# Kernel tuning notes

Hardware: AMD Instinct MI355X
Metric: run time of the kernel (lower is better)

Reference implementation:

```python
import jax, jax.numpy as jnp
import numpy as np

B, T_IN, T_DEC = 64, 64, 47   # batch, encoder len, decoder steps (max_length_output-1)
V, E, H = 32000, 512, 1024    # vocab, embed dim, hidden


def setup_inputs() -> dict:
    key = jax.random.key(0)
    ks = jax.random.split(key, 12)
    s = 0.02
    return {
        "tokens": jax.random.randint(ks[0], (B, T_DEC), 0, V),
        "memory": jax.random.normal(ks[1], (B, T_IN, H), jnp.float32),
        "enc_h": jax.random.normal(ks[2], (B, H), jnp.float32),
        "enc_c": jax.random.normal(ks[3], (B, H), jnp.float32),
        "emb": jax.random.normal(ks[4], (V, E), jnp.float32) * s,
        "Wm": jax.random.normal(ks[5], (H, H), jnp.float32) * s,      # Luong memory_layer (no bias)
        "Wa": jax.random.normal(ks[6], (2 * H, H), jnp.float32) * s,  # attention_layer (no bias)
        "lstm_k": jax.random.normal(ks[7], (E + H, 4 * H), jnp.float32) * s,
        "lstm_r": jax.random.normal(ks[8], (H, 4 * H), jnp.float32) * s,
        "lstm_b": jnp.zeros((4 * H,), jnp.float32),
        "fc_w": jax.random.normal(ks[9], (H, V), jnp.float32) * s,
        "fc_b": jnp.zeros((V,), jnp.float32),
    }


def reference(tokens, memory, enc_h, enc_c, emb, Wm, Wa, lstm_k, lstm_r, lstm_b, fc_w, fc_b):
    # Luong attention keys: memory projected once, outside the decode loop
    keys_att = jnp.einsum('bth,hu->btu', memory, Wm)          # [B,T_in,H]
    xs = jnp.swapaxes(emb[tokens], 0, 1)                      # [T_dec,B,E] teacher-forced inputs

    def step(carry, x_t):
        h, c, attn = carry
        # AttentionWrapper: cell input = concat(embedding, prev attention)
        inp = jnp.concatenate([x_t, attn], axis=-1)           # [B,E+H]
        z = inp @ lstm_k + h @ lstm_r + lstm_b                # [B,4H], Keras gate order i,f,g,o
        i, f, g, o = jnp.split(z, 4, axis=-1)
        c2 = jax.nn.sigmoid(f) * c + jax.nn.sigmoid(i) * jnp.tanh(g)
        h2 = jax.nn.sigmoid(o) * jnp.tanh(c2)
        # Luong score = query . keys; full-length memory (no mask needed)
        score = jnp.einsum('bh,bth->bt', h2, keys_att)        # [B,T_in]
        align = jax.nn.softmax(score, axis=-1)
        ctx = jnp.einsum('bt,bth->bh', align, memory)         # [B,H]
        attn2 = jnp.concatenate([h2, ctx], axis=-1) @ Wa      # attention_layer -> [B,H]
        logits = attn2 @ fc_w + fc_b                          # output_layer -> [B,V]
        return (h2, c2, attn2), logits

    init = (enc_h, enc_c, jnp.zeros_like(enc_h))
    _, ys = jax.lax.scan(step, init, xs)                      # [T_dec,B,V]
    return jnp.swapaxes(ys, 0, 1)                             # [B,T_dec,V]
```

## Files before the change

kernel.cpp:

```cpp
#include <hip/hip_runtime.h>

typedef __bf16 bf16;
typedef __bf16 bf16x8 __attribute__((ext_vector_type(8)));
typedef __bf16 bf16x4 __attribute__((ext_vector_type(4)));
typedef float  f32x4  __attribute__((ext_vector_type(4)));

__device__ __forceinline__ void async16(const bf16* g, bf16* l) {
  __builtin_amdgcn_global_load_lds(
      (__attribute__((address_space(1))) void*)(void*)(const_cast<bf16*>(g)),
      (__attribute__((address_space(3))) void*)(void*)l,
      16, 0, 0);
}


__global__ void cvt_bf16(const float* __restrict__ s, bf16* __restrict__ d, int n) {
  int i = blockIdx.x * blockDim.x + threadIdx.x;
  int stride = gridDim.x * blockDim.x;
  for (int k = i; k < n; k += stride) d[k] = (bf16)s[k];
}

__global__ void transpose_to_bf16(const float* __restrict__ src, bf16* __restrict__ dst,
                                  int R, int C) {
  __shared__ float tile[32][33];
  int c0 = blockIdx.x * 32, r0 = blockIdx.y * 32;
  int tx = threadIdx.x, ty = threadIdx.y;
#pragma unroll
  for (int k = 0; k < 32; k += 8)
    tile[ty + k][tx] = src[(size_t)(r0 + ty + k) * C + (c0 + tx)];
  __syncthreads();
#pragma unroll
  for (int k = 0; k < 32; k += 8)
    dst[(size_t)(c0 + ty + k) * R + (r0 + tx)] = (bf16)tile[tx][ty + k];
}

__global__ void gather_emb(const int* __restrict__ tokens, const float* __restrict__ emb,
                           bf16* __restrict__ X) {
  int r = blockIdx.x;
  int tid = threadIdx.x;
  if (r < 3008) {
    int t = r >> 6, b = r & 63;
    int tok = tokens[b * 47 + t];
    const float* e = emb + (size_t)tok * 512;
    for (int k = tid; k < 512; k += 128) X[(size_t)r * 512 + k] = (bf16)e[k];
  } else {
    for (int k = tid; k < 512; k += 128) X[(size_t)r * 512 + k] = (bf16)0.f;
  }
}

__global__ void init_state(const float* __restrict__ enc_h, const float* __restrict__ enc_c,
                           bf16* __restrict__ S0, float* __restrict__ cbuf) {
  int i = blockIdx.x * 256 + threadIdx.x;
  int b = i >> 10, u = i & 1023;
  S0[(size_t)b * 2048 + u]        = (bf16)enc_h[i];
  S0[(size_t)b * 2048 + 1024 + u] = (bf16)0.f;
  cbuf[i] = enc_c[i];
}

template <int MODE, int SWAP = 0>
__global__ __launch_bounds__(256) void gemm_bt(
    const bf16* __restrict__ A, int lda,
    const bf16* __restrict__ B, int ldb, int K,
    void* __restrict__ C, int ldc,
    const void* __restrict__ aux) {
  __shared__ bf16 As[128 * 32];
  __shared__ bf16 Bs[128 * 32];
  const int tid = threadIdx.x;
  const int wave = tid >> 6, lane = tid & 63;
  const int wm = wave >> 1, wn = wave & 1;
  const int quad = lane >> 4, l16 = lane & 15;
  const size_t r0 = (size_t)(SWAP ? blockIdx.x : blockIdx.y) * 128;
  const size_t c0 = (size_t)(SWAP ? blockIdx.y : blockIdx.x) * 128;

  f32x4 acc[4][4] = {};

  for (int k0 = 0; k0 < K; k0 += 32) {
#pragma unroll
    for (int j = 0; j < 2; ++j) {
      int seg = j * 256 + tid;
      int row = seg >> 2, ks = seg & 3;
      async16(A + (r0 + row) * (size_t)lda + k0 + ks * 8, As + seg * 8);
    }
#pragma unroll
    for (int j = 0; j < 2; ++j) {
      int seg = j * 256 + tid;
      int row = seg >> 2, ks = seg & 3;
      async16(B + (c0 + row) * (size_t)ldb + k0 + ks * 8, Bs + seg * 8);
    }
    __syncthreads();
    bf16x8 af[4], bfr[4];
#pragma unroll
    for (int mi = 0; mi < 4; ++mi)
      af[mi] = *(const bf16x8*)(As + (wm * 64 + mi * 16 + l16) * 32 + quad * 8);
#pragma unroll
    for (int ni = 0; ni < 4; ++ni)
      bfr[ni] = *(const bf16x8*)(Bs + (wn * 64 + ni * 16 + l16) * 32 + quad * 8);
#pragma unroll
    for (int mi = 0; mi < 4; ++mi)
#pragma unroll
      for (int ni = 0; ni < 4; ++ni)
        acc[mi][ni] = __builtin_amdgcn_mfma_f32_16x16x32_bf16(af[mi], bfr[ni], acc[mi][ni], 0, 0, 0);
    __syncthreads();
  }

#pragma unroll
  for (int mi = 0; mi < 4; ++mi)
#pragma unroll
    for (int ni = 0; ni < 4; ++ni)
#pragma unroll
      for (int reg = 0; reg < 4; ++reg) {
        size_t r = r0 + wm * 64 + mi * 16 + quad * 4 + reg;
        size_t c = c0 + wn * 64 + ni * 16 + l16;
        float v = acc[mi][ni][reg];
        if (MODE == 0) {
          ((bf16*)C)[r * ldc + c] = (bf16)v;
        } else if (MODE == 1) {
          if (c < 1024) v += (float)((const bf16*)aux)[r * 1024 + c];
          ((bf16*)C)[r * ldc + c] = (bf16)v;
        } else if (MODE == 2) {
          v += ((const float*)aux)[c];
          ((float*)C)[r * ldc + c] = v;
        } else if (MODE == 3) {
          if (r < 3008) {
            size_t t = r >> 6, b = r & 63;
            ((float*)C)[(b * 47 + t) * (size_t)32000 + c] = v + ((const float*)aux)[c];
          }
        } else {
          ((float*)C)[r * ldc + c] = v;
        }
      }
}

template <int KK>
__global__ __launch_bounds__(256) void step_gates2(
    const bf16* __restrict__ Sin,
    const bf16* __restrict__ Bt,
    int ldb,
    const float* __restrict__ pct,
    float* __restrict__ cbuf,
    bf16* __restrict__ HC_t)
{
  __shared__ bf16 Bs[16 * 2048];
  __shared__ float zs[64 * 16];
  const int tid = threadIdx.x;
  const int p = blockIdx.x;
  const int wave = tid >> 6, lane = tid & 63;
  const int quad = lane >> 4, l16 = lane & 15;

  constexpr int NSEG = KK / 8;
  constexpr int SH = (KK == 2048) ? 8 : 7;
#pragma unroll
  for (int i = 0; i < 16 * NSEG / 256; ++i) {
    int seg = i * 256 + tid;
    int n = seg >> SH;
    int ko = seg & (NSEG - 1);
    int gkb = (ko * 16) ^ ((n & 7) << 4);
    int ng = (n >> 2) * 1024 + p * 4 + (n & 3);
    async16(Bt + (size_t)ng * ldb + (gkb >> 1), Bs + n * 2048 + ko * 8);
  }

  const bf16* arow = Sin + (size_t)(wave * 16 + l16) * 2048 + quad * 8;
  const char* bbase = (const char*)Bs + l16 * 4096;
  const int bswz = (l16 & 7) << 4;
  __syncthreads();

  f32x4 acc0 = {}, acc1 = {};
  constexpr int KS = KK / 32;
#pragma unroll 8
  for (int ks = 0; ks < KS; ks += 2) {
    bf16x8 b0 = *(const bf16x8*)(bbase + ((ks * 64 + quad * 16) ^ bswz));
    bf16x8 a0 = *(const bf16x8*)(arow + (size_t)ks * 32);
    acc0 = __builtin_amdgcn_mfma_f32_16x16x32_bf16(a0, b0, acc0, 0, 0, 0);
    bf16x8 b1 = *(const bf16x8*)(bbase + (((ks + 1) * 64 + quad * 16) ^ bswz));
    bf16x8 a1 = *(const bf16x8*)(arow + (size_t)(ks + 1) * 32);
    acc1 = __builtin_amdgcn_mfma_f32_16x16x32_bf16(a1, b1, acc1, 0, 0, 0);
  }

  {
    int gcol = (l16 >> 2) * 1024 + p * 4 + (l16 & 3);
#pragma unroll
    for (int reg = 0; reg < 4; ++reg) {
      int row = wave * 16 + quad * 4 + reg;
      zs[row * 16 + l16] = acc0[reg] + acc1[reg] + pct[(size_t)row * 4096 + gcol];
    }
  }
  __syncthreads();

  {
    int b = tid >> 2, s = tid & 3;
    int j = p * 4 + s;
    float iv = zs[b * 16 + s];
    float fv = zs[b * 16 + 4 + s];
    float gv = zs[b * 16 + 8 + s];
    float ov = zs[b * 16 + 12 + s];
    float c_old = cbuf[b * 1024 + j];
    float ig = 1.f / (1.f + __expf(-iv));
    float fg = 1.f / (1.f + __expf(-fv));
    float og = 1.f / (1.f + __expf(-ov));
    float c2 = fg * c_old + ig * tanhf(gv);
    float h2 = og * tanhf(c2);
    cbuf[b * 1024 + j] = c2;
    HC_t[(size_t)b * 2048 + j] = (bf16)h2;
  }
}

__global__ __launch_bounds__(256) void step_attn2(
    bf16* __restrict__ HC_t,
    const float* __restrict__ keys,
    const bf16* __restrict__ memB)
{
  __shared__ float sm[64];
  const int b = blockIdx.x;
  const int tid = threadIdx.x;
  const int wave = tid >> 6, lane = tid & 63;

  float hv[16];
  {
    const bf16* hp = HC_t + (size_t)b * 2048 + lane * 16;
    bf16x8 h0 = *(const bf16x8*)(hp);
    bf16x8 h1 = *(const bf16x8*)(hp + 8);
#pragma unroll
    for (int e = 0; e < 8; ++e) { hv[e] = (float)h0[e]; hv[8 + e] = (float)h1[e]; }
  }

#pragma unroll 4
  for (int ii = 0; ii < 16; ++ii) {
    int it = wave * 16 + ii;
    const float* krow = keys + ((size_t)b * 64 + it) * 1024 + lane * 16;
    f32x4 k0 = *(const f32x4*)(krow);
    f32x4 k1 = *(const f32x4*)(krow + 4);
    f32x4 k2 = *(const f32x4*)(krow + 8);
    f32x4 k3 = *(const f32x4*)(krow + 12);
    float pr = hv[0] * k0[0] + hv[1] * k0[1] + hv[2] * k0[2] + hv[3] * k0[3]
             + hv[4] * k1[0] + hv[5] * k1[1] + hv[6] * k1[2] + hv[7] * k1[3]
             + hv[8] * k2[0] + hv[9] * k2[1] + hv[10] * k2[2] + hv[11] * k2[3]
             + hv[12] * k3[0] + hv[13] * k3[1] + hv[14] * k3[2] + hv[15] * k3[3];
#pragma unroll
    for (int off = 32; off > 0; off >>= 1) pr += __shfl_xor(pr, off);
    if (lane == 0) sm[it] = pr;
  }
  __syncthreads();

  if (tid < 64) {
    float s = sm[tid];
    float mx = s;
#pragma unroll
    for (int off = 32; off > 0; off >>= 1) mx = fmaxf(mx, __shfl_xor(mx, off));
    float e = __expf(s - mx);
    float sum = e;
#pragma unroll
    for (int off = 32; off > 0; off >>= 1) sum += __shfl_xor(sum, off);
    sm[tid] = e / sum;
  }
  __syncthreads();

  int u0 = tid * 4;
  float a0 = 0.f, a1 = 0.f, a2 = 0.f, a3 = 0.f;
#pragma unroll 4
  for (int i = 0; i < 64; ++i) {
    float al = sm[i];
    bf16x4 m4 = *(const bf16x4*)(memB + ((size_t)b * 64 + i) * 1024 + u0);
    a0 += al * (float)m4[0];
    a1 += al * (float)m4[1];
    a2 += al * (float)m4[2];
    a3 += al * (float)m4[3];
  }
  bf16* so = HC_t + (size_t)b * 2048 + 1024 + u0;
  so[0] = (bf16)a0;
  so[1] = (bf16)a1;
  so[2] = (bf16)a2;
  so[3] = (bf16)a3;
}


extern "C" void kernel_launch(void* const* d_in, const int* in_sizes, int n_in,
                              void* d_out, int out_size, void* d_ws, size_t ws_size,
                              hipStream_t stream) {
  const int*   tokens = (const int*)d_in[0];
  const float* memory = (const float*)d_in[1];
  const float* enc_h  = (const float*)d_in[2];
  const float* enc_c  = (const float*)d_in[3];
  const float* emb    = (const float*)d_in[4];
  const float* Wm     = (const float*)d_in[5];
  const float* Wa     = (const float*)d_in[6];
  const float* lstm_k = (const float*)d_in[7];
  const float* lstm_r = (const float*)d_in[8];
  const float* lstm_b = (const float*)d_in[9];
  const float* fc_w   = (const float*)d_in[10];
  const float* fc_b   = (const float*)d_in[11];
  float* out = (float*)d_out;

  char* ob = (char*)d_out;
  size_t off = 0;
  auto alloc_o = [&](size_t bytes) { char* q = ob + off; off += bytes; return q; };
  bf16*  memB    = (bf16*)alloc_o(8388608);
  float* keys    = (float*)alloc_o(16777216);
  bf16*  WaB     = (bf16*)alloc_o(4194304);
  bf16*  WmT     = (bf16*)alloc_o(2097152);
  bf16*  KpT     = (bf16*)alloc_o(8388608);
  bf16*  KxT     = (bf16*)alloc_o(4194304);
  bf16*  RT      = (bf16*)alloc_o(8388608);
  bf16*  WaT     = (bf16*)alloc_o(4194304);
  bf16*  X       = (bf16*)alloc_o(3145728);
  bf16*  W12T    = (bf16*)alloc_o(16777216);
  bf16*  S0      = (bf16*)alloc_o(262144);
  float* cbuf    = (float*)alloc_o(262144);
  bf16*  HC      = (bf16*)alloc_o(12582912);
  float* precomp = (float*)alloc_o(50331648);

  char* wb = (char*)d_ws;
  bf16* fcwT  = (bf16*)(wb);
  bf16* attnb = (bf16*)(wb + 65536000);

  dim3 tb(32, 8);

  cvt_bf16<<<2048, 256, 0, stream>>>(memory, memB, 4194304);
  cvt_bf16<<<2048, 256, 0, stream>>>(Wa, WaB, 2097152);
  transpose_to_bf16<<<dim3(32, 32), tb, 0, stream>>>(Wm, WmT, 1024, 1024);
  transpose_to_bf16<<<dim3(128, 32), tb, 0, stream>>>(lstm_k + (size_t)512 * 4096, KpT, 1024, 4096);
  transpose_to_bf16<<<dim3(128, 16), tb, 0, stream>>>(lstm_k, KxT, 512, 4096);
  transpose_to_bf16<<<dim3(128, 32), tb, 0, stream>>>(lstm_r, RT, 1024, 4096);
  transpose_to_bf16<<<dim3(32, 64), tb, 0, stream>>>(Wa, WaT, 2048, 1024);
  transpose_to_bf16<<<dim3(1000, 32), tb, 0, stream>>>(fc_w, fcwT, 1024, 32000);
  gather_emb<<<3072, 128, 0, stream>>>(tokens, emb, X);
  init_state<<<256, 256, 0, stream>>>(enc_h, enc_c, S0, cbuf);

  gemm_bt<4><<<dim3(8, 32), 256, 0, stream>>>(memB, 1024, WmT, 1024, 1024, keys, 1024, nullptr);
  gemm_bt<1><<<dim3(16, 32), 256, 0, stream>>>(KpT, 1024, WaB, 1024, 1024, W12T, 2048, RT);
  gemm_bt<2><<<dim3(32, 24), 256, 0, stream>>>(X, 512, KxT, 512, 512, precomp, 4096, lstm_b);

  for (int t = 0; t < 47; ++t) {
    const bf16* Sin = (t == 0) ? S0 : (HC + (size_t)(t - 1) * 131072);
    bf16* HC_t = HC + (size_t)t * 131072;
    const float* pct = precomp + (size_t)t * 262144;
    if (t == 0)
      step_gates2<1024><<<256, 256, 0, stream>>>(Sin, RT, 1024, pct, cbuf, HC_t);
    else
      step_gates2<2048><<<256, 256, 0, stream>>>(Sin, W12T, 2048, pct, cbuf, HC_t);
    step_attn2<<<64, 256, 0, stream>>>(HC_t, keys, memB);
  }

  gemm_bt<0><<<dim3(8, 24), 256, 0, stream>>>(HC, 2048, WaT, 2048, 2048, attnb, 1024, nullptr);
  gemm_bt<3, 1><<<dim3(24, 250), 256, 0, stream>>>(attnb, 1024, fcwT, 1024, 1024, out, 32000, fc_b);

  (void)in_sizes; (void)n_in; (void)out_size; (void)ws_size;
}
```

Measured before the change: 2.425 ms.

## Fuse decoder loop into one persistent kernel with atomic-flag grid barriers

Result: slower. 3.244 ms (+33.8%).

```diff
diff --git a/kernel.cpp b/kernel.cpp
--- a/kernel.cpp
+++ b/kernel.cpp
@@ -47,16 +47,16 @@
   }
 }
 
-__global__ void init_state(const float* __restrict__ enc_h, const float* __restrict__ enc_c,
-                           bf16* __restrict__ S0, float* __restrict__ cbuf) {
+__global__ void init_state(const float* __restrict__ enc_h, bf16* __restrict__ S0,
+                           unsigned int* __restrict__ flags) {
   int i = blockIdx.x * 256 + threadIdx.x;
   int b = i >> 10, u = i & 1023;
   S0[(size_t)b * 2048 + u]        = (bf16)enc_h[i];
   S0[(size_t)b * 2048 + 1024 + u] = (bf16)0.f;
-  cbuf[i] = enc_c[i];
-}
-
-template <int MODE, int SWAP = 0>
+  if (blockIdx.x == 0 && threadIdx.x < 128) flags[threadIdx.x] = 0u;
+}
+
+template <int MODE>
 __global__ __launch_bounds__(256) void gemm_bt(
     const bf16* __restrict__ A, int lda,
     const bf16* __restrict__ B, int ldb, int K,
@@ -68,8 +68,8 @@
   const int wave = tid >> 6, lane = tid & 63;
   const int wm = wave >> 1, wn = wave & 1;
   const int quad = lane >> 4, l16 = lane & 15;
-  const size_t r0 = (size_t)(SWAP ? blockIdx.x : blockIdx.y) * 128;
-  const size_t c0 = (size_t)(SWAP ? blockIdx.y : blockIdx.x) * 128;
+  const size_t r0 = (size_t)blockIdx.y * 128;
+  const size_t c0 = (size_t)blockIdx.x * 128;
 
   f32x4 acc[4][4] = {};
 
@@ -130,145 +130,186 @@
       }
 }
 
-template <int KK>
-__global__ __launch_bounds__(256) void step_gates2(
-    const bf16* __restrict__ Sin,
-    const bf16* __restrict__ Bt,
-    int ldb,
-    const float* __restrict__ pct,
-    float* __restrict__ cbuf,
-    bf16* __restrict__ HC_t)
+__global__ __launch_bounds__(256) void decoder_fused(
+    const bf16* __restrict__ S0,
+    const bf16* __restrict__ W12T,
+    const bf16* __restrict__ RT,
+    const float* __restrict__ precomp,
+    const float* __restrict__ enc_c,
+    const float* __restrict__ keys,
+    const bf16* __restrict__ memB,
+    bf16* __restrict__ HC,
+    unsigned int* __restrict__ flags)
 {
   __shared__ bf16 Bs[16 * 2048];
   __shared__ float zs[64 * 16];
+  __shared__ float sm[64];
+
   const int tid = threadIdx.x;
   const int p = blockIdx.x;
   const int wave = tid >> 6, lane = tid & 63;
   const int quad = lane >> 4, l16 = lane & 15;
-
-  constexpr int NSEG = KK / 8;
-  constexpr int SH = (KK == 2048) ? 8 : 7;
-#pragma unroll
-  for (int i = 0; i < 16 * NSEG / 256; ++i) {
+  const int growB = (l16 >> 2) * 1024 + p * 4 + (l16 & 3);
+
+#pragma unroll
+  for (int i = 0; i < 16; ++i) {
     int seg = i * 256 + tid;
-    int n = seg >> SH;
-    int ko = seg & (NSEG - 1);
+    int n = seg >> 8;
+    int ko = seg & 255;
     int gkb = (ko * 16) ^ ((n & 7) << 4);
     int ng = (n >> 2) * 1024 + p * 4 + (n & 3);
-    async16(Bt + (size_t)ng * ldb + (gkb >> 1), Bs + n * 2048 + ko * 8);
-  }
-
-  const bf16* arow = Sin + (size_t)(wave * 16 + l16) * 2048 + quad * 8;
+    async16(W12T + (size_t)ng * 2048 + (gkb >> 1), Bs + n * 2048 + ko * 8);
+  }
+
+  float c_reg;
+  {
+    int b = tid >> 2, s = tid & 3;
+    c_reg = enc_c[b * 1024 + p * 4 + s];
+  }
+
   const char* bbase = (const char*)Bs + l16 * 4096;
   const int bswz = (l16 & 7) << 4;
+
   __syncthreads();
 
-  f32x4 acc0 = {}, acc1 = {};
-  constexpr int KS = KK / 32;
+  for (int t = 0; t < 47; ++t) {
+    const bf16* Sin = t ? (HC + (size_t)(t - 1) * 131072) : S0;
+    bf16* HC_t = HC + (size_t)t * 131072;
+    const float* pct = precomp + (size_t)t * 262144;
+    const bf16* arow = Sin + (size_t)(wave * 16 + l16) * 2048 + quad * 8;
+
+    f32x4 acc0 = {}, acc1 = {};
+    if (t == 0) {
+      const bf16* brow = RT + (size_t)growB * 1024 + quad * 8;
 #pragma unroll 8
-  for (int ks = 0; ks < KS; ks += 2) {
-    bf16x8 b0 = *(const bf16x8*)(bbase + ((ks * 64 + quad * 16) ^ bswz));
-    bf16x8 a0 = *(const bf16x8*)(arow + (size_t)ks * 32);
-    acc0 = __builtin_amdgcn_mfma_f32_16x16x32_bf16(a0, b0, acc0, 0, 0, 0);
-    bf16x8 b1 = *(const bf16x8*)(bbase + (((ks + 1) * 64 + quad * 16) ^ bswz));
-    bf16x8 a1 = *(const bf16x8*)(arow + (size_t)(ks + 1) * 32);
-    acc1 = __builtin_amdgcn_mfma_f32_16x16x32_bf16(a1, b1, acc1, 0, 0, 0);
-  }
-
-  {
-    int gcol = (l16 >> 2) * 1024 + p * 4 + (l16 & 3);
+      for (int ks = 0; ks < 32; ks += 2) {
+        bf16x8 b0 = *(const bf16x8*)(brow + ks * 32);
+        bf16x8 a0 = *(const bf16x8*)(arow + (size_t)ks * 32);
+        acc0 = __builtin_amdgcn_mfma_f32_16x16x32_bf16(a0, b0, acc0, 0, 0, 0);
+        bf16x8 b1 = *(const bf16x8*)(brow + (ks + 1) * 32);
+        bf16x8 a1 = *(const bf16x8*)(arow + (size_t)(ks + 1) * 32);
+        acc1 = __builtin_amdgcn_mfma_f32_16x16x32_bf16(a1, b1, acc1, 0, 0, 0);
+      }
+    } else {
+#pragma unroll 8
+      for (int ks = 0; ks < 64; ks += 2) {
+        bf16x8 b0 = *(const bf16x8*)(bbase + ((ks * 64 + quad * 16) ^ bswz));
+        bf16x8 a0 = *(const bf16x8*)(arow + (size_t)ks * 32);
+        acc0 = __builtin_amdgcn_mfma_f32_16x16x32_bf16(a0, b0, acc0, 0, 0, 0);
+        bf16x8 b1 = *(const bf16x8*)(bbase + (((ks + 1) * 64 + quad * 16) ^ bswz));
+        bf16x8 a1 = *(const bf16x8*)(arow + (size_t)(ks + 1) * 32);
+        acc1 = __builtin_amdgcn_mfma_f32_16x16x32_bf16(a1, b1, acc1, 0, 0, 0);
+      }
+    }
+
 #pragma unroll
     for (int reg = 0; reg < 4; ++reg) {
       int row = wave * 16 + quad * 4 + reg;
-      zs[row * 16 + l16] = acc0[reg] + acc1[reg] + pct[(size_t)row * 4096 + gcol];
-    }
-  }
-  __syncthreads();
-
-  {
-    int b = tid >> 2, s = tid & 3;
-    int j = p * 4 + s;
-    float iv = zs[b * 16 + s];
-    float fv = zs[b * 16 + 4 + s];
-    float gv = zs[b * 16 + 8 + s];
-    float ov = zs[b * 16 + 12 + s];
-    float c_old = cbuf[b * 1024 + j];
-    float ig = 1.f / (1.f + __expf(-iv));
-    float fg = 1.f / (1.f + __expf(-fv));
-    float og = 1.f / (1.f + __expf(-ov));
-    float c2 = fg * c_old + ig * tanhf(gv);
-    float h2 = og * tanhf(c2);
-    cbuf[b * 1024 + j] = c2;
-    HC_t[(size_t)b * 2048 + j] = (bf16)h2;
-  }
-}
-
-__global__ __launch_bounds__(256) void step_attn2(
-    bf16* __restrict__ HC_t,
-    const float* __restrict__ keys,
-    const bf16* __restrict__ memB)
-{
-  __shared__ float sm[64];
-  const int b = blockIdx.x;
-  const int tid = threadIdx.x;
-  const int wave = tid >> 6, lane = tid & 63;
-
-  float hv[16];
-  {
-    const bf16* hp = HC_t + (size_t)b * 2048 + lane * 16;
-    bf16x8 h0 = *(const bf16x8*)(hp);
-    bf16x8 h1 = *(const bf16x8*)(hp + 8);
-#pragma unroll
-    for (int e = 0; e < 8; ++e) { hv[e] = (float)h0[e]; hv[8 + e] = (float)h1[e]; }
-  }
+      zs[row * 16 + l16] = acc0[reg] + acc1[reg] + pct[(size_t)row * 4096 + growB];
+    }
+    __syncthreads();
+
+    {
+      int b = tid >> 2, s = tid & 3;
+      float iv = zs[b * 16 + s];
+      float fv = zs[b * 16 + 4 + s];
+      float gv = zs[b * 16 + 8 + s];
+      float ov = zs[b * 16 + 12 + s];
+      float ig = 1.f / (1.f + __expf(-iv));
+      float fg = 1.f / (1.f + __expf(-fv));
+      float og = 1.f / (1.f + __expf(-ov));
+      float c2 = fg * c_reg + ig * tanhf(gv);
+      float h2 = og * tanhf(c2);
+      c_reg = c2;
+      HC_t[(size_t)b * 2048 + p * 4 + s] = (bf16)h2;
+    }
+    __syncthreads();
+    if (tid == 0) {
+      __threadfence();
+      __hip_atomic_fetch_add(&flags[t], 1u, __ATOMIC_RELAXED, __HIP_MEMORY_SCOPE_AGENT);
+    }
+
+    if (p < 64) {
+      if (tid == 0) {
+        while (__hip_atomic_load(&flags[t], __ATOMIC_RELAXED, __HIP_MEMORY_SCOPE_AGENT) < 256u)
+          __builtin_amdgcn_s_sleep(2);
+        __threadfence();
+      }
+      __syncthreads();
+
+      const int b = p;
+      float hv[16];
+      {
+        const bf16* hp = HC_t + (size_t)b * 2048 + lane * 16;
+        bf16x8 h0 = *(const bf16x8*)(hp);
+        bf16x8 h1 = *(const bf16x8*)(hp + 8);
+#pragma unroll
+        for (int e = 0; e < 8; ++e) { hv[e] = (float)h0[e]; hv[8 + e] = (float)h1[e]; }
+      }
 
 #pragma unroll 4
-  for (int ii = 0; ii < 16; ++ii) {
-    int it = wave * 16 + ii;
-    const float* krow = keys + ((size_t)b * 64 + it) * 1024 + lane * 16;
-    f32x4 k0 = *(const f32x4*)(krow);
-    f32x4 k1 = *(const f32x4*)(krow + 4);
-    f32x4 k2 = *(const f32x4*)(krow + 8);
-    f32x4 k3 = *(const f32x4*)(krow + 12);
-    float pr = hv[0] * k0[0] + hv[1] * k0[1] + hv[2] * k0[2] + hv[3] * k0[3]
-             + hv[4] * k1[0] + hv[5] * k1[1] + hv[6] * k1[2] + hv[7] * k1[3]
-             + hv[8] * k2[0] + hv[9] * k2[1] + hv[10] * k2[2] + hv[11] * k2[3]
-             + hv[12] * k3[0] + hv[13] * k3[1] + hv[14] * k3[2] + hv[15] * k3[3];
-#pragma unroll
-    for (int off = 32; off > 0; off >>= 1) pr += __shfl_xor(pr, off);
-    if (lane == 0) sm[it] = pr;
-  }
-  __syncthreads();
-
-  if (tid < 64) {
-    float s = sm[tid];
-    float mx = s;
-#pragma unroll
-    for (int off = 32; off > 0; off >>= 1) mx = fmaxf(mx, __shfl_xor(mx, off));
-    float e = __expf(s - mx);
-    float sum = e;
-#pragma unroll
-    for (int off = 32; off > 0; off >>= 1) sum += __shfl_xor(sum, off);
-    sm[tid] = e / sum;
-  }
-  __syncthreads();
-
-  int u0 = tid * 4;
-  float a0 = 0.f, a1 = 0.f, a2 = 0.f, a3 = 0.f;
+      for (int ii = 0; ii < 16; ++ii) {
+        int it = wave * 16 + ii;
+        const float* krow = keys + ((size_t)b * 64 + it) * 1024 + lane * 16;
+        f32x4 k0 = *(const f32x4*)(krow);
+        f32x4 k1 = *(const f32x4*)(krow + 4);
+        f32x4 k2 = *(const f32x4*)(krow + 8);
+        f32x4 k3 = *(const f32x4*)(krow + 12);
+        float pr = hv[0] * k0[0] + hv[1] * k0[1] + hv[2] * k0[2] + hv[3] * k0[3]
+                 + hv[4] * k1[0] + hv[5] * k1[1] + hv[6] * k1[2] + hv[7] * k1[3]
+                 + hv[8] * k2[0] + hv[9] * k2[1] + hv[10] * k2[2] + hv[11] * k2[3]
+                 + hv[12] * k3[0] + hv[13] * k3[1] + hv[14] * k3[2] + hv[15] * k3[3];
+#pragma unroll
+        for (int off = 32; off > 0; off >>= 1) pr += __shfl_xor(pr, off);
+        if (lane == 0) sm[it] = pr;
+      }
+      __syncthreads();
+
+      if (tid < 64) {
+        float s = sm[tid];
+        float mx = s;
+#pragma unroll
+        for (int off = 32; off > 0; off >>= 1) mx = fmaxf(mx, __shfl_xor(mx, off));
+        float e = __expf(s - mx);
+        float sum = e;
+#pragma unroll
+        for (int off = 32; off > 0; off >>= 1) sum += __shfl_xor(sum, off);
+        sm[tid] = e / sum;
+      }
+      __syncthreads();
+
+      int u0 = tid * 4;
+      float a0 = 0.f, a1 = 0.f, a2 = 0.f, a3 = 0.f;
 #pragma unroll 4
-  for (int i = 0; i < 64; ++i) {
-    float al = sm[i];
-    bf16x4 m4 = *(const bf16x4*)(memB + ((size_t)b * 64 + i) * 1024 + u0);
-    a0 += al * (float)m4[0];
-    a1 += al * (float)m4[1];
-    a2 += al * (float)m4[2];
-    a3 += al * (float)m4[3];
-  }
-  bf16* so = HC_t + (size_t)b * 2048 + 1024 + u0;
-  so[0] = (bf16)a0;
-  so[1] = (bf16)a1;
-  so[2] = (bf16)a2;
-  so[3] = (bf16)a3;
+      for (int i = 0; i < 64; ++i) {
+        float al = sm[i];
+        bf16x4 m4 = *(const bf16x4*)(memB + ((size_t)b * 64 + i) * 1024 + u0);
+        a0 += al * (float)m4[0];
+        a1 += al * (float)m4[1];
+        a2 += al * (float)m4[2];
+        a3 += al * (float)m4[3];
+      }
+      bf16* so = HC_t + (size_t)b * 2048 + 1024 + u0;
+      so[0] = (bf16)a0;
+      so[1] = (bf16)a1;
+      so[2] = (bf16)a2;
+      so[3] = (bf16)a3;
+      __syncthreads();
+      if (tid == 0) {
+        __threadfence();
+        __hip_atomic_fetch_add(&flags[64 + t], 1u, __ATOMIC_RELAXED, __HIP_MEMORY_SCOPE_AGENT);
+      }
+    }
+
+    if (t < 46) {
+      if (tid == 0) {
+        while (__hip_atomic_load(&flags[64 + t], __ATOMIC_RELAXED, __HIP_MEMORY_SCOPE_AGENT) < 64u)
+          __builtin_amdgcn_s_sleep(2);
+        __threadfence();
+      }
+      __syncthreads();
+    }
+  }
 }
 
 
@@ -303,9 +344,9 @@
   bf16*  X       = (bf16*)alloc_o(3145728);
   bf16*  W12T    = (bf16*)alloc_o(16777216);
   bf16*  S0      = (bf16*)alloc_o(262144);
-  float* cbuf    = (float*)alloc_o(262144);
   bf16*  HC      = (bf16*)alloc_o(12582912);
   float* precomp = (float*)alloc_o(50331648);
+  unsigned int* flags = (unsigned int*)alloc_o(512);
 
   char* wb = (char*)d_ws;
   bf16* fcwT  = (bf16*)(wb);
@@ -322,25 +363,16 @@
   transpose_to_bf16<<<dim3(32, 64), tb, 0, stream>>>(Wa, WaT, 2048, 1024);
   transpose_to_bf16<<<dim3(1000, 32), tb, 0, stream>>>(fc_w, fcwT, 1024, 32000);
   gather_emb<<<3072, 128, 0, stream>>>(tokens, emb, X);
-  init_state<<<256, 256, 0, stream>>>(enc_h, enc_c, S0, cbuf);
+  init_state<<<256, 256, 0, stream>>>(enc_h, S0, flags);
 
   gemm_bt<4><<<dim3(8, 32), 256, 0, stream>>>(memB, 1024, WmT, 1024, 1024, keys, 1024, nullptr);
   gemm_bt<1><<<dim3(16, 32), 256, 0, stream>>>(KpT, 1024, WaB, 1024, 1024, W12T, 2048, RT);
   gemm_bt<2><<<dim3(32, 24), 256, 0, stream>>>(X, 512, KxT, 512, 512, precomp, 4096, lstm_b);
 
-  for (int t = 0; t < 47; ++t) {
-    const bf16* Sin = (t == 0) ? S0 : (HC + (size_t)(t - 1) * 131072);
-    bf16* HC_t = HC + (size_t)t * 131072;
-    const float* pct = precomp + (size_t)t * 262144;
-    if (t == 0)
-      step_gates2<1024><<<256, 256, 0, stream>>>(Sin, RT, 1024, pct, cbuf, HC_t);
-    else
-      step_gates2<2048><<<256, 256, 0, stream>>>(Sin, W12T, 2048, pct, cbuf, HC_t);
-    step_attn2<<<64, 256, 0, stream>>>(HC_t, keys, memB);
-  }
+  decoder_fused<<<256, 256, 0, stream>>>(S0, W12T, RT, precomp, enc_c, keys, memB, HC, flags);
 
   gemm_bt<0><<<dim3(8, 24), 256, 0, stream>>>(HC, 2048, WaT, 2048, 2048, attnb, 1024, nullptr);
-  gemm_bt<3, 1><<<dim3(24, 250), 256, 0, stream>>>(attnb, 1024, fcwT, 1024, 1024, out, 32000, fc_b);
+  gemm_bt<3><<<dim3(250, 24), 256, 0, stream>>>(attnb, 1024, fcwT, 1024, 1024, out, 32000, fc_b);
 
   (void)in_sizes; (void)n_in; (void)out_size; (void)ws_size;
 }
```
